# Kernel optimization log

Measured on AMD Instinct MI355X. Metric: run time of the kernel, lower is better.

The kernel has to match this reference:

```python
import jax, jax.numpy as jnp
import numpy as np

DEPTH = 4
DIM = 1024
HEADS = 16
DIM_HEAD = 64
INNER = HEADS * DIM_HEAD  # 1024
MLP = 4096
CTX = 768
SCALE = DIM_HEAD ** -0.5
EPS = 1e-5


def setup_inputs() -> dict:
    key = jax.random.key(0)
    ks = jax.random.split(key, 12)
    def rn(k, shape, s=0.02):
        return jax.random.normal(k, shape, jnp.float32) * s
    return {
        "x": jax.random.normal(ks[0], (2, 2048, DIM), jnp.float32),
        "context": jax.random.normal(ks[1], (2, 1024, CTX), jnp.float32),
        "ln1_g": jnp.ones((DEPTH, DIM), jnp.float32),
        "ln1_b": jnp.zeros((DEPTH, DIM), jnp.float32),
        "w_qkv": rn(ks[2], (DEPTH, DIM, 3 * INNER)),
        "w_sa_o": rn(ks[3], (DEPTH, INNER, DIM)),
        "b_sa_o": jnp.zeros((DEPTH, DIM), jnp.float32),
        "ln2_g": jnp.ones((DEPTH, DIM), jnp.float32),
        "ln2_b": jnp.zeros((DEPTH, DIM), jnp.float32),
        "w_q": rn(ks[4], (DEPTH, DIM, INNER)),
        "w_kv": rn(ks[5], (DEPTH, CTX, 2 * INNER)),
        "w_ca_o": rn(ks[6], (DEPTH, INNER, DIM)),
        "b_ca_o": jnp.zeros((DEPTH, DIM), jnp.float32),
        "ln3_g": jnp.ones((DEPTH, DIM), jnp.float32),
        "ln3_b": jnp.zeros((DEPTH, DIM), jnp.float32),
        "w_ff1": rn(ks[7], (DEPTH, DIM, MLP)),
        "b_ff1": jnp.zeros((DEPTH, MLP), jnp.float32),
        "w_ff2": rn(ks[8], (DEPTH, MLP, DIM)),
        "b_ff2": jnp.zeros((DEPTH, DIM), jnp.float32),
    }


def _ln(x, g, b):
    mu = jnp.mean(x, axis=-1, keepdims=True)
    var = jnp.mean(jnp.square(x - mu), axis=-1, keepdims=True)
    return (x - mu) * jax.lax.rsqrt(var + EPS) * g + b


def _heads(t):
    # [b, n, h*d] -> [b, h, n, d]
    b, n, _ = t.shape
    return t.reshape(b, n, HEADS, DIM_HEAD).transpose(0, 2, 1, 3)


def _mha(q, k, v):
    # q,k,v: [b, h, n, d]; naive matmul-softmax-matmul, same math as the torch code
    attn = jax.nn.softmax(jnp.einsum('bhqd,bhkd->bhqk', q, k) * SCALE, axis=-1)
    out = jnp.einsum('bhqk,bhkd->bhqd', attn, v)
    b, h, n, d = out.shape
    return out.transpose(0, 2, 1, 3).reshape(b, n, h * d)


def reference(x, context, ln1_g, ln1_b, w_qkv, w_sa_o, b_sa_o,
              ln2_g, ln2_b, w_q, w_kv, w_ca_o, b_ca_o,
              ln3_g, ln3_b, w_ff1, b_ff1, w_ff2, b_ff2):
    for i in range(DEPTH):
        # self-attention
        h = _ln(x, ln1_g[i], ln1_b[i])
        qkv = h @ w_qkv[i]
        q, k, v = jnp.split(qkv, 3, axis=-1)
        sa = _mha(_heads(q), _heads(k), _heads(v)) @ w_sa_o[i] + b_sa_o[i]
        x = sa + x
        # cross-attention
        h = _ln(x, ln2_g[i], ln2_b[i])
        q = h @ w_q[i]
        kv = context @ w_kv[i]
        k, v = jnp.split(kv, 2, axis=-1)
        ca = _mha(_heads(q), _heads(k), _heads(v)) @ w_ca_o[i] + b_ca_o[i]
        x = ca + x
        # feed-forward (exact GELU, matching torch nn.GELU default)
        h = _ln(x, ln3_g[i], ln3_b[i])
        ff = jax.nn.gelu(h @ w_ff1[i] + b_ff1[i], approximate=False) @ w_ff2[i] + b_ff2[i]
        x = ff + x
    return x
```

## Files before the change

### kernel.cpp

```cpp
#include <hip/hip_runtime.h>
#include <hip/hip_bf16.h>
#include <math.h>

typedef __bf16 bf16_t;
typedef __bf16 bf16x8 __attribute__((ext_vector_type(8)));
typedef __bf16 bf16x4 __attribute__((ext_vector_type(4)));
typedef float f32x4 __attribute__((ext_vector_type(4)));
typedef float f32x16 __attribute__((ext_vector_type(16)));
typedef unsigned short u16;
typedef unsigned int u32;
typedef u16 u16x8 __attribute__((ext_vector_type(8)));
typedef u32 u32x4 __attribute__((ext_vector_type(4)));

#define NDEPTH 4
#define DIM 1024
#define NHEADS 16
#define MLP_DIM 4096
#define CTXD 768
#define NTOK 4096
#define NCTX 2048
#define ATT_SC2 0.18033688011112042f

__device__ inline void gload_lds16(const void* g, void* l) {
  __builtin_amdgcn_global_load_lds(
      (const __attribute__((address_space(1))) void*)g,
      (__attribute__((address_space(3))) void*)l, 16, 0, 0);
}

__device__ inline u32 packbf2(float a, float b) {
  union { bf16_t h[2]; u32 w; } u;
  u.h[0] = (bf16_t)a; u.h[1] = (bf16_t)b;
  return u.w;
}

__device__ inline void xcd_swizzle(int& bx, int& by) {
  const int gx = gridDim.x, nwg = gx * gridDim.y;
  int id = by * gx + bx;
  id = (id & 7) * (nwg >> 3) + (id >> 3);
  bx = id % gx; by = id / gx;
}

template<int EPI>
__device__ inline void epi_store(void* outp, const float* bias, const float* res,
                                 int row, int col, int N, float v) {
  size_t idx = (size_t)row * N + col;
  if (EPI == 3) {
    ((float*)outp)[idx] = v + bias[col] + res[idx];
  } else if (EPI == 2) {
    float vb = v + bias[col];
    ((bf16_t*)outp)[idx] = (bf16_t)(0.5f * vb * (1.f + erff(vb * 0.70710678118f)));
  } else {
    ((bf16_t*)outp)[idx] = (bf16_t)v;
  }
}

__device__ inline int swz_slot(int row, int slot) { return slot ^ ((row >> 1) & 3); }

template<int EPI>
__global__ __launch_bounds__(512) void gemm_bf16(
    const bf16_t* __restrict__ A, const bf16_t* __restrict__ Bt,
    const float* __restrict__ bias, const float* __restrict__ res,
    void* __restrict__ outp, int M, int N, int K)
{
  __shared__ alignas(16) bf16_t As[3 * 128 * 32];
  __shared__ alignas(16) bf16_t Bs[3 * 128 * 32];
  const int tid = threadIdx.x, lane = tid & 63, wave = tid >> 6;
  int bx = blockIdx.x, by = blockIdx.y;
  xcd_swizzle(bx, by);
  const int wr = wave >> 2, wc = wave & 3;
  const int l15 = lane & 15, l4 = lane >> 4;

  const int srow = tid >> 2;
  const int soff = swz_slot(srow, tid & 3) * 8;
  const bf16_t* gA = A + (size_t)by * 128 * K + (size_t)srow * K + soff;
  const bf16_t* gB = Bt + (size_t)bx * 128 * K + (size_t)srow * K + soff;
  bf16_t* lA = &As[tid * 8];
  bf16_t* lB = &Bs[tid * 8];

  f32x4 acc[4][2] = {};

  int aoff[4], boff[2];
#pragma unroll
  for (int mi = 0; mi < 4; ++mi) {
    int row = wr * 64 + mi * 16 + l15;
    aoff[mi] = row * 32 + swz_slot(row, l4) * 8;
  }
#pragma unroll
  for (int ni = 0; ni < 2; ++ni) {
    int row = wc * 32 + ni * 16 + l15;
    boff[ni] = row * 32 + swz_slot(row, l4) * 8;
  }

  auto compute = [&](int cur) {
    bf16x8 af[4], bfr[2];
#pragma unroll
    for (int mi = 0; mi < 4; ++mi)
      af[mi] = *(const bf16x8*)&As[cur * 4096 + aoff[mi]];
#pragma unroll
    for (int ni = 0; ni < 2; ++ni)
      bfr[ni] = *(const bf16x8*)&Bs[cur * 4096 + boff[ni]];
#pragma unroll
    for (int mi = 0; mi < 4; ++mi)
#pragma unroll
      for (int ni = 0; ni < 2; ++ni)
        acc[mi][ni] = __builtin_amdgcn_mfma_f32_16x16x32_bf16(af[mi], bfr[ni], acc[mi][ni], 0, 0, 0);
  };

  const int nk = K >> 5;

  gload_lds16(gA, lA);            gload_lds16(gB, lB);
  gload_lds16(gA + 32, lA + 4096); gload_lds16(gB + 32, lB + 4096);
  asm volatile("s_waitcnt vmcnt(2)" ::: "memory");
  __builtin_amdgcn_s_barrier();
  __builtin_amdgcn_sched_barrier(0);
  gA += 64; gB += 64;

  const int ngroups = (nk - 2) / 3;
  for (int j = 0; j < ngroups; ++j) {
#pragma unroll
    for (int r = 0; r < 3; ++r) {
      gload_lds16(gA + r * 32, lA + ((r + 2) % 3) * 4096);
      gload_lds16(gB + r * 32, lB + ((r + 2) % 3) * 4096);
      compute(r);
      asm volatile("s_waitcnt vmcnt(2)" ::: "memory");
      __builtin_amdgcn_s_barrier();
      __builtin_amdgcn_sched_barrier(0);
    }
    gA += 96; gB += 96;
  }
  compute(0);
  asm volatile("s_waitcnt vmcnt(0)" ::: "memory");
  __builtin_amdgcn_s_barrier();
  __builtin_amdgcn_sched_barrier(0);
  compute(1);

  const int r0 = by * 128 + wr * 64, c0 = bx * 128 + wc * 32;
#pragma unroll
  for (int ni = 0; ni < 2; ++ni)
#pragma unroll
    for (int mi = 0; mi < 4; ++mi)
#pragma unroll
      for (int r = 0; r < 4; ++r)
        epi_store<EPI>(outp, bias, res, r0 + mi * 16 + l4 * 4 + r,
                       c0 + ni * 16 + l15, N, acc[mi][ni][r]);
}

template<int EPI>
__global__ __launch_bounds__(256) void gemm64_bf16(
    const bf16_t* __restrict__ A, const bf16_t* __restrict__ Bt,
    const float* __restrict__ bias, const float* __restrict__ res,
    void* __restrict__ outp, int M, int N, int K)
{
  __shared__ alignas(16) bf16_t As[4 * 64 * 32];
  __shared__ alignas(16) bf16_t Bs[4 * 64 * 32];
  const int tid = threadIdx.x, lane = tid & 63, wave = tid >> 6;
  int bx = blockIdx.x, by = blockIdx.y;
  xcd_swizzle(bx, by);
  const int wr = wave >> 1, wc = wave & 1;
  const int l15 = lane & 15, l4 = lane >> 4;

  const int srow = tid >> 2;
  const int soff = swz_slot(srow, tid & 3) * 8;
  const bf16_t* gA = A + (size_t)by * 64 * K + (size_t)srow * K + soff;
  const bf16_t* gB = Bt + (size_t)bx * 64 * K + (size_t)srow * K + soff;
  bf16_t* lA = &As[tid * 8];
  bf16_t* lB = &Bs[tid * 8];

  f32x4 acc[2][2] = {};

  int aoff[2], boff[2];
#pragma unroll
  for (int mi = 0; mi < 2; ++mi) {
    int row = wr * 32 + mi * 16 + l15;
    aoff[mi] = row * 32 + swz_slot(row, l4) * 8;
  }
#pragma unroll
  for (int ni = 0; ni < 2; ++ni) {
    int row = wc * 32 + ni * 16 + l15;
    boff[ni] = row * 32 + swz_slot(row, l4) * 8;
  }

  auto compute = [&](int cur) {
    bf16x8 af[2], bfr[2];
#pragma unroll
    for (int mi = 0; mi < 2; ++mi)
      af[mi] = *(const bf16x8*)&As[cur * 2048 + aoff[mi]];
#pragma unroll
    for (int ni = 0; ni < 2; ++ni)
      bfr[ni] = *(const bf16x8*)&Bs[cur * 2048 + boff[ni]];
#pragma unroll
    for (int mi = 0; mi < 2; ++mi)
#pragma unroll
      for (int ni = 0; ni < 2; ++ni)
        acc[mi][ni] = __builtin_amdgcn_mfma_f32_16x16x32_bf16(af[mi], bfr[ni], acc[mi][ni], 0, 0, 0);
  };

  const int nk = K >> 5;

  gload_lds16(gA, lA);            gload_lds16(gB, lB);
  gload_lds16(gA + 32, lA + 2048); gload_lds16(gB + 32, lB + 2048);
  asm volatile("s_waitcnt vmcnt(2)" ::: "memory");
  __builtin_amdgcn_s_barrier();
  __builtin_amdgcn_sched_barrier(0);
  gA += 64; gB += 64;

  for (int j = 0; j < (nk >> 2) - 1; ++j) {
#pragma unroll
    for (int r = 0; r < 4; ++r) {
      gload_lds16(gA + r * 32, lA + ((r + 2) & 3) * 2048);
      gload_lds16(gB + r * 32, lB + ((r + 2) & 3) * 2048);
      compute(r);
      asm volatile("s_waitcnt vmcnt(2)" ::: "memory");
      __builtin_amdgcn_s_barrier();
      __builtin_amdgcn_sched_barrier(0);
    }
    gA += 128; gB += 128;
  }
  gload_lds16(gA, lA + 2 * 2048);
  gload_lds16(gB, lB + 2 * 2048);
  compute(0);
  asm volatile("s_waitcnt vmcnt(2)" ::: "memory");
  __builtin_amdgcn_s_barrier();
  __builtin_amdgcn_sched_barrier(0);
  gload_lds16(gA + 32, lA + 3 * 2048);
  gload_lds16(gB + 32, lB + 3 * 2048);
  compute(1);
  asm volatile("s_waitcnt vmcnt(2)" ::: "memory");
  __builtin_amdgcn_s_barrier();
  __builtin_amdgcn_sched_barrier(0);
  compute(2);
  asm volatile("s_waitcnt vmcnt(0)" ::: "memory");
  __builtin_amdgcn_s_barrier();
  __builtin_amdgcn_sched_barrier(0);
  compute(3);

  const int r0 = by * 64 + wr * 32, c0 = bx * 64 + wc * 32;
#pragma unroll
  for (int ni = 0; ni < 2; ++ni)
#pragma unroll
    for (int mi = 0; mi < 2; ++mi)
#pragma unroll
      for (int r = 0; r < 4; ++r)
        epi_store<EPI>(outp, bias, res, r0 + mi * 16 + l4 * 4 + r,
                       c0 + ni * 16 + l15, N, acc[mi][ni][r]);
}

__global__ void v_transpose(const bf16_t* __restrict__ V, int vs,
                            bf16_t* __restrict__ out, int nk)
{
  __shared__ u16 t[32][33];
  const int z = blockIdx.z;
  const int b = z >> 4, h = z & 15;
  const bf16_t* src = V + (size_t)b * nk * vs + h * 64;
  bf16_t* dst = out + (size_t)z * 64 * nk;
  const int k0 = blockIdx.x * 32, d0 = blockIdx.y * 32;
  const int tx = threadIdx.x, ty = threadIdx.y;
#pragma unroll
  for (int i = ty; i < 32; i += 8)
    t[i][tx] = *(const u16*)(src + (size_t)(k0 + i) * vs + d0 + tx);
  __syncthreads();
#pragma unroll
  for (int i = ty; i < 32; i += 8)
    *(u16*)(dst + (size_t)(d0 + i) * nk + k0 + tx) = t[tx][i];
}

__global__ __launch_bounds__(256, 4) void attn_fwd(
    const bf16_t* __restrict__ Q, int qs,
    const bf16_t* __restrict__ K, int ks,
    const bf16_t* __restrict__ Vt,
    bf16_t* __restrict__ O, int os, int nq, int nk)
{
  __shared__ alignas(16) bf16_t Ks[2][64][72];
  __shared__ alignas(16) bf16_t Vs[2][64][72];

  const int tid = threadIdx.x, lane = tid & 63, wv = tid >> 6;
  const int l31 = lane & 31, hi = lane >> 5;
  const int pair = wv >> 1, sK = wv & 1;
  const int h = blockIdx.y, bz = blockIdx.z;
  const size_t qrow0 = (size_t)bz * nq + (size_t)blockIdx.x * 64 + pair * 32;
  const bf16_t* Qb = Q + qrow0 * qs + h * 64;
  const bf16_t* Kb = K + (size_t)bz * nk * ks + h * 64;
  const bf16_t* Vb = Vt + (size_t)(bz * 16 + h) * 64 * nk;
  bf16_t* Ob = O + qrow0 * os + h * 64;

  bf16x8 qa[4];
#pragma unroll
  for (int c = 0; c < 4; ++c) {
    bf16x8 t = *(const bf16x8*)(Qb + (size_t)l31 * qs + c * 16 + hi * 8);
#pragma unroll
    for (int j = 0; j < 8; ++j)
      qa[c][j] = (bf16_t)((float)t[j] * ATT_SC2);
  }

  u16x8 kreg[2], vreg[2];
  auto load_tile = [&](int kt) {
#pragma unroll
    for (int i = 0; i < 2; ++i) {
      int lin = i * 256 + tid, row = lin >> 3, col = (lin & 7) * 8;
      kreg[i] = *(const u16x8*)(Kb + (size_t)(kt * 64 + row) * ks + col);
      vreg[i] = *(const u16x8*)(Vb + (size_t)row * nk + kt * 64 + col);
    }
  };
  auto store_tile = [&](int buf) {
#pragma unroll
    for (int i = 0; i < 2; ++i) {
      int lin = i * 256 + tid, row = lin >> 3, col = (lin & 7) * 8;
      *(u16x8*)&Ks[buf][row][col] = kreg[i];
      *(u16x8*)&Vs[buf][row][col] = vreg[i];
    }
  };

  f32x16 acc[2] = {};
  f32x16 lacc = {};

  const bf16_t onev = (bf16_t)1.0f;
  const bf16x8 vones = {onev, onev, onev, onev, onev, onev, onev, onev};

  const int nt = nk >> 6;
  load_tile(0);
  store_tile(0);
  __syncthreads();

  for (int kt = 0; kt < nt; ++kt) {
    const int cur = kt & 1;
    const bool pre = (kt + 1 < nt);
    if (pre) load_tile(kt + 1);

    f32x16 s = {};
    __builtin_amdgcn_s_setprio(1);
#pragma unroll
    for (int c = 0; c < 4; ++c) {
      bf16x8 kf = *(const bf16x8*)&Ks[cur][sK * 32 + l31][c * 16 + hi * 8];
      s = __builtin_amdgcn_mfma_f32_32x32x16_bf16(kf, qa[c], s, 0, 0, 0);
    }
    __builtin_amdgcn_s_setprio(0);

    u32x4 paw[2];
#pragma unroll
    for (int h2 = 0; h2 < 2; ++h2) {
      u32 a0 = packbf2(exp2f(s[h2 * 8 + 0]), exp2f(s[h2 * 8 + 1]));
      u32 a1 = packbf2(exp2f(s[h2 * 8 + 2]), exp2f(s[h2 * 8 + 3]));
      u32 a2 = packbf2(exp2f(s[h2 * 8 + 4]), exp2f(s[h2 * 8 + 5]));
      u32 a3 = packbf2(exp2f(s[h2 * 8 + 6]), exp2f(s[h2 * 8 + 7]));
      asm volatile("v_permlane32_swap_b32 %0, %1" : "+v"(a0), "+v"(a2));
      asm volatile("v_permlane32_swap_b32 %0, %1" : "+v"(a1), "+v"(a3));
      paw[h2][0] = a0; paw[h2][1] = a1; paw[h2][2] = a2; paw[h2][3] = a3;
    }

    __builtin_amdgcn_s_setprio(1);
#pragma unroll
    for (int h2 = 0; h2 < 2; ++h2) {
      union { u32x4 w; bf16x8 v; } pu;
      pu.w = paw[h2];
      lacc = __builtin_amdgcn_mfma_f32_32x32x16_bf16(pu.v, vones, lacc, 0, 0, 0);
#pragma unroll
      for (int dblk = 0; dblk < 2; ++dblk) {
        bf16x8 vb = *(const bf16x8*)&Vs[cur][dblk * 32 + l31][sK * 32 + h2 * 16 + hi * 8];
        acc[dblk] = __builtin_amdgcn_mfma_f32_32x32x16_bf16(pu.v, vb, acc[dblk], 0, 0, 0);
      }
    }
    __builtin_amdgcn_s_setprio(0);

    if (pre) store_tile(cur ^ 1);
    __syncthreads();
  }

  float* mb = (float*)&Ks[0][0][0];
  float* ml = (float*)&Vs[0][0][0];
  if (sK == 1) {
#pragma unroll
    for (int dblk = 0; dblk < 2; ++dblk)
#pragma unroll
      for (int r = 0; r < 16; ++r)
        mb[((pair * 2 + dblk) * 16 + r) * 64 + lane] = acc[dblk][r];
#pragma unroll
    for (int r = 0; r < 16; ++r)
      ml[(pair * 16 + r) * 64 + lane] = lacc[r];
  }
  __syncthreads();
  if (sK == 0) {
#pragma unroll
    for (int r = 0; r < 16; ++r) {
      int q = (r & 3) + 8 * (r >> 2) + 4 * hi;
      float inv = 1.f / (lacc[r] + ml[(pair * 16 + r) * 64 + lane]);
#pragma unroll
      for (int dblk = 0; dblk < 2; ++dblk) {
        float o = (acc[dblk][r] + mb[((pair * 2 + dblk) * 16 + r) * 64 + lane]) * inv;
        Ob[(size_t)q * os + dblk * 32 + l31] = (bf16_t)o;
      }
    }
  }
}

__global__ __launch_bounds__(256) void layernorm_f32_bf16(
    const float* __restrict__ x, const float* __restrict__ g, const float* __restrict__ b,
    bf16_t* __restrict__ out)
{
  const int row = blockIdx.x, tid = threadIdx.x;
  const float4 v = ((const float4*)(x + (size_t)row * 1024))[tid];
  float s = v.x + v.y + v.z + v.w;
  float s2 = v.x * v.x + v.y * v.y + v.z * v.z + v.w * v.w;
#pragma unroll
  for (int off = 32; off > 0; off >>= 1) {
    s += __shfl_down(s, off);
    s2 += __shfl_down(s2, off);
  }
  __shared__ float ps[4], ps2[4];
  const int lane = tid & 63, wave = tid >> 6;
  if (lane == 0) { ps[wave] = s; ps2[wave] = s2; }
  __syncthreads();
  s = ps[0] + ps[1] + ps[2] + ps[3];
  s2 = ps2[0] + ps2[1] + ps2[2] + ps2[3];
  const float mu = s * (1.f / 1024.f);
  const float var = s2 * (1.f / 1024.f) - mu * mu;
  const float rstd = rsqrtf(var + 1e-5f);
  const float4 gv = ((const float4*)g)[tid];
  const float4 bv = ((const float4*)b)[tid];
  bf16x4 o;
  o[0] = (bf16_t)((v.x - mu) * rstd * gv.x + bv.x);
  o[1] = (bf16_t)((v.y - mu) * rstd * gv.y + bv.y);
  o[2] = (bf16_t)((v.z - mu) * rstd * gv.z + bv.z);
  o[3] = (bf16_t)((v.w - mu) * rstd * gv.w + bv.w);
  *(bf16x4*)(out + (size_t)row * 1024 + tid * 4) = o;
}

__global__ void transpose_to_bf16(const float* __restrict__ src, bf16_t* __restrict__ dst, int K, int N)
{
  __shared__ float tile[32][33];
  const size_t loff = (size_t)blockIdx.z * K * N;
  src += loff; dst += loff;
  const int k0 = blockIdx.y * 32, n0 = blockIdx.x * 32;
  const int tx = threadIdx.x, ty = threadIdx.y;
#pragma unroll
  for (int i = ty; i < 32; i += 8)
    tile[i][tx] = src[(size_t)(k0 + i) * N + n0 + tx];
  __syncthreads();
#pragma unroll
  for (int i = ty; i < 32; i += 8)
    dst[(size_t)(n0 + i) * K + k0 + tx] = (bf16_t)tile[tx][i];
}

__global__ void f32_to_bf16(const float* __restrict__ src, bf16_t* __restrict__ dst, int n4)
{
  int i = blockIdx.x * blockDim.x + threadIdx.x;
  if (i < n4) {
    float4 v = ((const float4*)src)[i];
    bf16x4 o;
    o[0] = (bf16_t)v.x; o[1] = (bf16_t)v.y; o[2] = (bf16_t)v.z; o[3] = (bf16_t)v.w;
    ((bf16x4*)dst)[i] = o;
  }
}

__global__ void copy_f32(const float* __restrict__ src, float* __restrict__ dst, int n4)
{
  int i = blockIdx.x * blockDim.x + threadIdx.x;
  if (i < n4) ((float4*)dst)[i] = ((const float4*)src)[i];
}

extern "C" void kernel_launch(void* const* d_in, const int* in_sizes, int n_in,
                              void* d_out, int out_size, void* d_ws, size_t ws_size,
                              hipStream_t stream)
{
  const float* x      = (const float*)d_in[0];
  const float* ctx    = (const float*)d_in[1];
  const float* ln1_g  = (const float*)d_in[2];
  const float* ln1_b  = (const float*)d_in[3];
  const float* w_qkv  = (const float*)d_in[4];
  const float* w_sa_o = (const float*)d_in[5];
  const float* b_sa_o = (const float*)d_in[6];
  const float* ln2_g  = (const float*)d_in[7];
  const float* ln2_b  = (const float*)d_in[8];
  const float* w_q    = (const float*)d_in[9];
  const float* w_kv   = (const float*)d_in[10];
  const float* w_ca_o = (const float*)d_in[11];
  const float* b_ca_o = (const float*)d_in[12];
  const float* ln3_g  = (const float*)d_in[13];
  const float* ln3_b  = (const float*)d_in[14];
  const float* w_ff1  = (const float*)d_in[15];
  const float* b_ff1  = (const float*)d_in[16];
  const float* w_ff2  = (const float*)d_in[17];
  const float* b_ff2  = (const float*)d_in[18];

  char* p = (char*)d_ws;
  auto alloc = [&](size_t bytes) { char* r = p; p += (bytes + 255) & ~(size_t)255; return r; };
  bf16_t* wqkv_t = (bf16_t*)alloc((size_t)NDEPTH * 3072 * 1024 * 2);
  bf16_t* wsao_t = (bf16_t*)alloc((size_t)NDEPTH * 1024 * 1024 * 2);
  bf16_t* wq_t   = (bf16_t*)alloc((size_t)NDEPTH * 1024 * 1024 * 2);
  bf16_t* wkv_t  = (bf16_t*)alloc((size_t)NDEPTH * 2048 * 768 * 2);
  bf16_t* wcao_t = (bf16_t*)alloc((size_t)NDEPTH * 1024 * 1024 * 2);
  bf16_t* wff1_t = (bf16_t*)alloc((size_t)NDEPTH * 4096 * 1024 * 2);
  bf16_t* wff2_t = (bf16_t*)alloc((size_t)NDEPTH * 1024 * 4096 * 2);
  bf16_t* ctxb   = (bf16_t*)alloc((size_t)NCTX * CTXD * 2);
  float*  xbuf   = (float*)alloc((size_t)NTOK * DIM * 4);
  bf16_t* lnbuf  = (bf16_t*)alloc((size_t)NTOK * DIM * 2);
  bf16_t* bigbuf = (bf16_t*)alloc((size_t)NTOK * 4096 * 2);
  bf16_t* qbuf   = (bf16_t*)alloc((size_t)NTOK * DIM * 2);
  bf16_t* kvbuf  = (bf16_t*)alloc((size_t)NCTX * 2048 * 2);
  bf16_t* vtbuf  = (bf16_t*)alloc((size_t)32 * 64 * 2048 * 2);
  bf16_t* vtcbuf = (bf16_t*)alloc((size_t)32 * 64 * 1024 * 2);
  if ((size_t)(p - (char*)d_ws) > ws_size) return;

  dim3 tb(32, 8);
  transpose_to_bf16<<<dim3(3072 / 32, 1024 / 32, NDEPTH), tb, 0, stream>>>(w_qkv, wqkv_t, 1024, 3072);
  transpose_to_bf16<<<dim3(1024 / 32, 1024 / 32, NDEPTH), tb, 0, stream>>>(w_sa_o, wsao_t, 1024, 1024);
  transpose_to_bf16<<<dim3(1024 / 32, 1024 / 32, NDEPTH), tb, 0, stream>>>(w_q, wq_t, 1024, 1024);
  transpose_to_bf16<<<dim3(2048 / 32, 768 / 32, NDEPTH), tb, 0, stream>>>(w_kv, wkv_t, 768, 2048);
  transpose_to_bf16<<<dim3(1024 / 32, 1024 / 32, NDEPTH), tb, 0, stream>>>(w_ca_o, wcao_t, 1024, 1024);
  transpose_to_bf16<<<dim3(4096 / 32, 1024 / 32, NDEPTH), tb, 0, stream>>>(w_ff1, wff1_t, 1024, 4096);
  transpose_to_bf16<<<dim3(1024 / 32, 4096 / 32, NDEPTH), tb, 0, stream>>>(w_ff2, wff2_t, 4096, 1024);
  f32_to_bf16<<<(NCTX * CTXD / 4 + 255) / 256, 256, 0, stream>>>(ctx, ctxb, NCTX * CTXD / 4);
  copy_f32<<<(NTOK * DIM / 4 + 255) / 256, 256, 0, stream>>>(x, xbuf, NTOK * DIM / 4);

  for (int i = 0; i < NDEPTH; ++i) {
    layernorm_f32_bf16<<<NTOK, 256, 0, stream>>>(xbuf, ln1_g + i * DIM, ln1_b + i * DIM, lnbuf);
    gemm_bf16<0><<<dim3(3072 / 128, NTOK / 128), 512, 0, stream>>>(
        lnbuf, wqkv_t + (size_t)i * 3072 * 1024, nullptr, nullptr, bigbuf, NTOK, 3072, 1024);
    v_transpose<<<dim3(2048 / 32, 2, 32), tb, 0, stream>>>(bigbuf + 2048, 3072, vtbuf, 2048);
    attn_fwd<<<dim3(2048 / 64, NHEADS, 2), 256, 0, stream>>>(
        bigbuf, 3072, bigbuf + 1024, 3072, vtbuf, lnbuf, 1024, 2048, 2048);
    gemm64_bf16<3><<<dim3(1024 / 64, NTOK / 64), 256, 0, stream>>>(
        lnbuf, wsao_t + (size_t)i * 1024 * 1024, b_sa_o + i * DIM, xbuf, xbuf, NTOK, 1024, 1024);
    layernorm_f32_bf16<<<NTOK, 256, 0, stream>>>(xbuf, ln2_g + i * DIM, ln2_b + i * DIM, lnbuf);
    gemm64_bf16<0><<<dim3(1024 / 64, NTOK / 64), 256, 0, stream>>>(
        lnbuf, wq_t + (size_t)i * 1024 * 1024, nullptr, nullptr, qbuf, NTOK, 1024, 1024);
    gemm64_bf16<0><<<dim3(2048 / 64, NCTX / 64), 256, 0, stream>>>(
        ctxb, wkv_t + (size_t)i * 2048 * 768, nullptr, nullptr, kvbuf, NCTX, 2048, 768);
    v_transpose<<<dim3(1024 / 32, 2, 32), tb, 0, stream>>>(kvbuf + 1024, 2048, vtcbuf, 1024);
    attn_fwd<<<dim3(2048 / 64, NHEADS, 2), 256, 0, stream>>>(
        qbuf, 1024, kvbuf, 2048, vtcbuf, lnbuf, 1024, 2048, 1024);
    gemm64_bf16<3><<<dim3(1024 / 64, NTOK / 64), 256, 0, stream>>>(
        lnbuf, wcao_t + (size_t)i * 1024 * 1024, b_ca_o + i * DIM, xbuf, xbuf, NTOK, 1024, 1024);
    layernorm_f32_bf16<<<NTOK, 256, 0, stream>>>(xbuf, ln3_g + i * DIM, ln3_b + i * DIM, lnbuf);
    gemm_bf16<2><<<dim3(4096 / 128, NTOK / 128), 512, 0, stream>>>(
        lnbuf, wff1_t + (size_t)i * 4096 * 1024, b_ff1 + i * MLP_DIM, nullptr, bigbuf, NTOK, 4096, 1024);
    gemm64_bf16<3><<<dim3(1024 / 64, NTOK / 64), 256, 0, stream>>>(
        bigbuf, wff2_t + (size_t)i * 1024 * 4096, b_ff2 + i * DIM, xbuf, xbuf, NTOK, 1024, 4096);
  }
  copy_f32<<<(NTOK * DIM / 4 + 255) / 256, 256, 0, stream>>>(xbuf, (float*)d_out, NTOK * DIM / 4);
}
```

Measured before the change: 1.581 ms.

## Load attention K/V fragments straight from global memory, dropping LDS staging

The attention kernel no longer stages K and V tiles through double-buffered shared memory with per-tile barriers. Each wave now loads the exact MFMA operand fragments it needs directly from global memory into registers, so the main loop needs no __syncthreads. The launch-bounds occupancy hint is also removed. The cost is that the two wave pairs sharing a K half now each fetch it, relying on cache, and there is no explicit prefetch, so global load latency may be exposed to the MFMA chain.

```diff
diff --git a/kernel.cpp b/kernel.cpp
--- a/kernel.cpp
+++ b/kernel.cpp
@@ -264,14 +264,14 @@
     *(u16*)(dst + (size_t)(d0 + i) * nk + k0 + tx) = t[tx][i];
 }
 
-__global__ __launch_bounds__(256, 4) void attn_fwd(
+__global__ __launch_bounds__(256) void attn_fwd(
     const bf16_t* __restrict__ Q, int qs,
     const bf16_t* __restrict__ K, int ks,
     const bf16_t* __restrict__ Vt,
     bf16_t* __restrict__ O, int os, int nq, int nk)
 {
-  __shared__ alignas(16) bf16_t Ks[2][64][72];
-  __shared__ alignas(16) bf16_t Vs[2][64][72];
+  __shared__ float mb[2][2][16][64];
+  __shared__ float ml[2][16][64];
 
   const int tid = threadIdx.x, lane = tid & 63, wv = tid >> 6;
   const int l31 = lane & 31, hi = lane >> 5;
@@ -292,23 +292,10 @@
       qa[c][j] = (bf16_t)((float)t[j] * ATT_SC2);
   }
 
-  u16x8 kreg[2], vreg[2];
-  auto load_tile = [&](int kt) {
-#pragma unroll
-    for (int i = 0; i < 2; ++i) {
-      int lin = i * 256 + tid, row = lin >> 3, col = (lin & 7) * 8;
-      kreg[i] = *(const u16x8*)(Kb + (size_t)(kt * 64 + row) * ks + col);
-      vreg[i] = *(const u16x8*)(Vb + (size_t)row * nk + kt * 64 + col);
-    }
-  };
-  auto store_tile = [&](int buf) {
-#pragma unroll
-    for (int i = 0; i < 2; ++i) {
-      int lin = i * 256 + tid, row = lin >> 3, col = (lin & 7) * 8;
-      *(u16x8*)&Ks[buf][row][col] = kreg[i];
-      *(u16x8*)&Vs[buf][row][col] = vreg[i];
-    }
-  };
+  const bf16_t* kp  = Kb + (size_t)(sK * 32 + l31) * ks + hi * 8;
+  const bf16_t* vp0 = Vb + (size_t)l31 * nk + sK * 32 + hi * 8;
+  const bf16_t* vp1 = vp0 + (size_t)32 * nk;
+  const size_t kbump = (size_t)64 * ks;
 
   f32x16 acc[2] = {};
   f32x16 lacc = {};
@@ -317,22 +304,22 @@
   const bf16x8 vones = {onev, onev, onev, onev, onev, onev, onev, onev};
 
   const int nt = nk >> 6;
-  load_tile(0);
-  store_tile(0);
-  __syncthreads();
-
   for (int kt = 0; kt < nt; ++kt) {
-    const int cur = kt & 1;
-    const bool pre = (kt + 1 < nt);
-    if (pre) load_tile(kt + 1);
+    bf16x8 kf[4], vb0[2], vb1[2];
+#pragma unroll
+    for (int c = 0; c < 4; ++c) kf[c] = *(const bf16x8*)(kp + c * 16);
+#pragma unroll
+    for (int h2 = 0; h2 < 2; ++h2) {
+      vb0[h2] = *(const bf16x8*)(vp0 + h2 * 16);
+      vb1[h2] = *(const bf16x8*)(vp1 + h2 * 16);
+    }
+    kp += kbump; vp0 += 64; vp1 += 64;
 
     f32x16 s = {};
     __builtin_amdgcn_s_setprio(1);
 #pragma unroll
-    for (int c = 0; c < 4; ++c) {
-      bf16x8 kf = *(const bf16x8*)&Ks[cur][sK * 32 + l31][c * 16 + hi * 8];
-      s = __builtin_amdgcn_mfma_f32_32x32x16_bf16(kf, qa[c], s, 0, 0, 0);
-    }
+    for (int c = 0; c < 4; ++c)
+      s = __builtin_amdgcn_mfma_f32_32x32x16_bf16(kf[c], qa[c], s, 0, 0, 0);
     __builtin_amdgcn_s_setprio(0);
 
     u32x4 paw[2];
@@ -353,39 +340,31 @@
       union { u32x4 w; bf16x8 v; } pu;
       pu.w = paw[h2];
       lacc = __builtin_amdgcn_mfma_f32_32x32x16_bf16(pu.v, vones, lacc, 0, 0, 0);
-#pragma unroll
-      for (int dblk = 0; dblk < 2; ++dblk) {
-        bf16x8 vb = *(const bf16x8*)&Vs[cur][dblk * 32 + l31][sK * 32 + h2 * 16 + hi * 8];
-        acc[dblk] = __builtin_amdgcn_mfma_f32_32x32x16_bf16(pu.v, vb, acc[dblk], 0, 0, 0);
-      }
+      acc[0] = __builtin_amdgcn_mfma_f32_32x32x16_bf16(pu.v, vb0[h2], acc[0], 0, 0, 0);
+      acc[1] = __builtin_amdgcn_mfma_f32_32x32x16_bf16(pu.v, vb1[h2], acc[1], 0, 0, 0);
     }
     __builtin_amdgcn_s_setprio(0);
-
-    if (pre) store_tile(cur ^ 1);
-    __syncthreads();
-  }
-
-  float* mb = (float*)&Ks[0][0][0];
-  float* ml = (float*)&Vs[0][0][0];
+  }
+
   if (sK == 1) {
 #pragma unroll
     for (int dblk = 0; dblk < 2; ++dblk)
 #pragma unroll
       for (int r = 0; r < 16; ++r)
-        mb[((pair * 2 + dblk) * 16 + r) * 64 + lane] = acc[dblk][r];
+        mb[pair][dblk][r][lane] = acc[dblk][r];
 #pragma unroll
     for (int r = 0; r < 16; ++r)
-      ml[(pair * 16 + r) * 64 + lane] = lacc[r];
+      ml[pair][r][lane] = lacc[r];
   }
   __syncthreads();
   if (sK == 0) {
 #pragma unroll
     for (int r = 0; r < 16; ++r) {
       int q = (r & 3) + 8 * (r >> 2) + 4 * hi;
-      float inv = 1.f / (lacc[r] + ml[(pair * 16 + r) * 64 + lane]);
+      float inv = 1.f / (lacc[r] + ml[pair][r][lane]);
 #pragma unroll
       for (int dblk = 0; dblk < 2; ++dblk) {
-        float o = (acc[dblk][r] + mb[((pair * 2 + dblk) * 16 + r) * 64 + lane]) * inv;
+        float o = (acc[dblk][r] + mb[pair][dblk][r][lane]) * inv;
         Ob[(size_t)q * os + dblk * 32 + l31] = (bf16_t)o;
       }
     }
```

Measured after the change: 2.050 ms. 1.3x slower.

## Stage attention K/V tiles via direct global-to-LDS loads with XOR swizzle

Applied to the files above, without the earlier changes.

Replaces the register-staged K/V tile copy in the attention kernel with global_load_lds direct transfers into double-buffered LDS. The padded 72-wide layout is swapped for an unpadded 64-wide layout with an XOR swizzle to avoid bank conflicts. The aim is to cut VGPR pressure and the copy instructions, so the prefetch overlaps with MFMA work. The launch-bounds occupancy hint is also dropped. It relies on manual vmcnt waits and raw barriers, and a wrong wait or swizzle would give incorrect results.

```diff
diff --git a/kernel.cpp b/kernel.cpp
--- a/kernel.cpp
+++ b/kernel.cpp
@@ -55,6 +55,7 @@
 }
 
 __device__ inline int swz_slot(int row, int slot) { return slot ^ ((row >> 1) & 3); }
+__device__ inline int swz8(int row, int slot) { return slot ^ ((row >> 1) & 7); }
 
 template<int EPI>
 __global__ __launch_bounds__(512) void gemm_bf16(
@@ -264,14 +265,14 @@
     *(u16*)(dst + (size_t)(d0 + i) * nk + k0 + tx) = t[tx][i];
 }
 
-__global__ __launch_bounds__(256, 4) void attn_fwd(
+__global__ __launch_bounds__(256) void attn_fwd(
     const bf16_t* __restrict__ Q, int qs,
     const bf16_t* __restrict__ K, int ks,
     const bf16_t* __restrict__ Vt,
     bf16_t* __restrict__ O, int os, int nq, int nk)
 {
-  __shared__ alignas(16) bf16_t Ks[2][64][72];
-  __shared__ alignas(16) bf16_t Vs[2][64][72];
+  __shared__ alignas(16) bf16_t Ks[2 * 64 * 64];
+  __shared__ alignas(16) bf16_t Vs[2 * 64 * 64];
 
   const int tid = threadIdx.x, lane = tid & 63, wv = tid >> 6;
   const int l31 = lane & 31, hi = lane >> 5;
@@ -292,23 +293,36 @@
       qa[c][j] = (bf16_t)((float)t[j] * ATT_SC2);
   }
 
-  u16x8 kreg[2], vreg[2];
-  auto load_tile = [&](int kt) {
-#pragma unroll
-    for (int i = 0; i < 2; ++i) {
-      int lin = i * 256 + tid, row = lin >> 3, col = (lin & 7) * 8;
-      kreg[i] = *(const u16x8*)(Kb + (size_t)(kt * 64 + row) * ks + col);
-      vreg[i] = *(const u16x8*)(Vb + (size_t)row * nk + kt * 64 + col);
-    }
+  const int srow0 = tid >> 3, sslot0 = tid & 7;
+  const int srow1 = (256 + tid) >> 3, sslot1 = tid & 7;
+  const bf16_t* gK0 = Kb + (size_t)srow0 * ks + swz8(srow0, sslot0) * 8;
+  const bf16_t* gK1 = Kb + (size_t)srow1 * ks + swz8(srow1, sslot1) * 8;
+  const bf16_t* gV0 = Vb + (size_t)srow0 * nk + swz8(srow0, sslot0) * 8;
+  const bf16_t* gV1 = Vb + (size_t)srow1 * nk + swz8(srow1, sslot1) * 8;
+  bf16_t* lK = &Ks[tid * 8];
+  bf16_t* lV = &Vs[tid * 8];
+  const size_t kstep = (size_t)64 * ks;
+
+  auto stage = [&](int kt, int buf) {
+    gload_lds16(gK0 + (size_t)kt * kstep, lK + buf * 4096);
+    gload_lds16(gK1 + (size_t)kt * kstep, lK + buf * 4096 + 2048);
+    gload_lds16(gV0 + kt * 64, lV + buf * 4096);
+    gload_lds16(gV1 + kt * 64, lV + buf * 4096 + 2048);
   };
-  auto store_tile = [&](int buf) {
-#pragma unroll
-    for (int i = 0; i < 2; ++i) {
-      int lin = i * 256 + tid, row = lin >> 3, col = (lin & 7) * 8;
-      *(u16x8*)&Ks[buf][row][col] = kreg[i];
-      *(u16x8*)&Vs[buf][row][col] = vreg[i];
-    }
-  };
+
+  int koff[4], voff[2][2];
+#pragma unroll
+  for (int c = 0; c < 4; ++c) {
+    int row = sK * 32 + l31;
+    koff[c] = row * 64 + swz8(row, 2 * c + hi) * 8;
+  }
+#pragma unroll
+  for (int dblk = 0; dblk < 2; ++dblk)
+#pragma unroll
+    for (int h2 = 0; h2 < 2; ++h2) {
+      int row = dblk * 32 + l31;
+      voff[dblk][h2] = row * 64 + swz8(row, sK * 4 + h2 * 2 + hi) * 8;
+    }
 
   f32x16 acc[2] = {};
   f32x16 lacc = {};
@@ -317,20 +331,21 @@
   const bf16x8 vones = {onev, onev, onev, onev, onev, onev, onev, onev};
 
   const int nt = nk >> 6;
-  load_tile(0);
-  store_tile(0);
-  __syncthreads();
+  stage(0, 0);
+  asm volatile("s_waitcnt vmcnt(0)" ::: "memory");
+  __builtin_amdgcn_s_barrier();
+  __builtin_amdgcn_sched_barrier(0);
 
   for (int kt = 0; kt < nt; ++kt) {
     const int cur = kt & 1;
     const bool pre = (kt + 1 < nt);
-    if (pre) load_tile(kt + 1);
+    if (pre) stage(kt + 1, cur ^ 1);
 
     f32x16 s = {};
     __builtin_amdgcn_s_setprio(1);
 #pragma unroll
     for (int c = 0; c < 4; ++c) {
-      bf16x8 kf = *(const bf16x8*)&Ks[cur][sK * 32 + l31][c * 16 + hi * 8];
+      bf16x8 kf = *(const bf16x8*)&Ks[cur * 4096 + koff[c]];
       s = __builtin_amdgcn_mfma_f32_32x32x16_bf16(kf, qa[c], s, 0, 0, 0);
     }
     __builtin_amdgcn_s_setprio(0);
@@ -355,18 +370,19 @@
       lacc = __builtin_amdgcn_mfma_f32_32x32x16_bf16(pu.v, vones, lacc, 0, 0, 0);
 #pragma unroll
       for (int dblk = 0; dblk < 2; ++dblk) {
-        bf16x8 vb = *(const bf16x8*)&Vs[cur][dblk * 32 + l31][sK * 32 + h2 * 16 + hi * 8];
+        bf16x8 vb = *(const bf16x8*)&Vs[cur * 4096 + voff[dblk][h2]];
         acc[dblk] = __builtin_amdgcn_mfma_f32_32x32x16_bf16(pu.v, vb, acc[dblk], 0, 0, 0);
       }
     }
     __builtin_amdgcn_s_setprio(0);
 
-    if (pre) store_tile(cur ^ 1);
-    __syncthreads();
-  }
-
-  float* mb = (float*)&Ks[0][0][0];
-  float* ml = (float*)&Vs[0][0][0];
+    if (pre) { asm volatile("s_waitcnt vmcnt(0)" ::: "memory"); }
+    __builtin_amdgcn_s_barrier();
+    __builtin_amdgcn_sched_barrier(0);
+  }
+
+  float* mb = (float*)&Ks[0];
+  float* ml = (float*)&Vs[0];
   if (sK == 1) {
 #pragma unroll
     for (int dblk = 0; dblk < 2; ++dblk)
```

New measurement: 1.623 ms. +2.7%, slower.
